# Performance work log

Measured on AMD Instinct MI355X. Metric: run time of the kernel, lower is better.

## Reference

```python
import jax, jax.numpy as jnp
import numpy as np
from jax import lax

# LRN hyperparameters (from module __init__)
K = 2.0
KERNEL = 5
ALPHA = 1e-4
BETA = 0.75
PAD = KERNEL // 2


def setup_inputs() -> dict:
    key = jax.random.key(0)
    x = jax.random.normal(key, (16, 96, 224, 224), dtype=jnp.float32)
    return {"x": x}


def reference(x) -> jnp.ndarray:
    # Spatial local response norm: per-channel k x k box sum of squares
    # (equivalent to Unfold(kernel, pad=kernel//2) -> view -> square -> sum over window).
    sq = x * x
    ssq = lax.reduce_window(
        sq,
        jnp.float32(0.0),
        lax.add,
        window_dimensions=(1, 1, KERNEL, KERNEL),
        window_strides=(1, 1, 1, 1),
        padding=((0, 0), (0, 0), (PAD, PAD), (PAD, PAD)),
    )
    denom = (K + ALPHA * ssq) ** BETA
    return x / denom
```

## Files before the change

kernel.cpp:

```cpp
#include <hip/hip_runtime.h>


typedef float f4 __attribute__((ext_vector_type(4)));

#define LRN_H 224
#define LRN_W 224
#define LRN_WQ 56
#define LRN_R 4
#define LRN_IN (LRN_R + 4)
#define LRN_SLABS (LRN_H / LRN_R)
#define LRN_PLANE (LRN_H * LRN_W)

__global__ __launch_bounds__(256, 6) void LocalResponseNorm_17420387352942_kernel(
        const float* __restrict__ x, float* __restrict__ out) {
    const int q    = threadIdx.x & 63;
    const int wave = threadIdx.x >> 6;
    const int job  = blockIdx.x * 4 + wave;
    const int plane = job / LRN_SLABS;
    const int slab  = job - plane * LRN_SLABS;
    const int h0    = slab * LRN_R;

    const int qe = min(q, LRN_WQ - 1);
    const float* __restrict__ px = x   + (size_t)plane * LRN_PLANE + (qe << 2);
    float* __restrict__       po = out + (size_t)plane * LRN_PLANE + (qe << 2);

    const bool okL = (qe > 0);
    const bool okR = (qe < LRN_WQ - 1);
    const bool wr  = (q < LRN_WQ);

    f4 X[LRN_IN];
#pragma unroll
    for (int r = 0; r < LRN_IN; ++r) {
        const int row = h0 + r - 2;
        const int rc  = min(max(row, 0), LRN_H - 1);
        X[r] = *(const f4*)(px + rc * LRN_W);
    }

    f4 acc[LRN_R];
#pragma unroll
    for (int i = 0; i < LRN_R; ++i) acc[i] = (f4){0.f, 0.f, 0.f, 0.f};

#pragma unroll
    for (int r = 0; r < LRN_IN; ++r) {
        const int row = h0 + r - 2;
        const float mV = (row >= 0 && row < LRN_H) ? 1.0f : 0.0f;
        f4 sq = X[r] * X[r];
        sq *= mV;

        float a  = __shfl_up(sq[2], 1);
        float b  = __shfl_up(sq[3], 1);
        float d0 = __shfl_down(sq[0], 1);
        float d1 = __shfl_down(sq[1], 1);
        a  = okL ? a  : 0.0f;
        b  = okL ? b  : 0.0f;
        d0 = okR ? d0 : 0.0f;
        d1 = okR ? d1 : 0.0f;

        float t = sq[1] + sq[2];
        f4 rs;
        rs[0] = a + b + sq[0] + t;
        rs[1] = b + sq[0] + t + sq[3];
        rs[2] = sq[0] + t + sq[3] + d0;
        rs[3] = t + sq[3] + d0 + d1;

#pragma unroll
        for (int i = 0; i < LRN_R; ++i) {
            if (i <= r && r <= i + 4) acc[i] += rs;
        }
    }

#pragma unroll
    for (int i = 0; i < LRN_R; ++i) {
        f4 o;
#pragma unroll
        for (int j = 0; j < 4; ++j) {
            float d   = fmaf(1e-4f, acc[i][j], 2.0f);
            float rsq = __builtin_amdgcn_rsqf(d);
            o[j] = X[i + 2][j] * rsq * __builtin_amdgcn_sqrtf(rsq);
        }
        if (wr) __builtin_nontemporal_store(o, (f4*)(po + (h0 + i) * LRN_W));
    }
}

extern "C" void kernel_launch(void* const* d_in, const int* in_sizes, int n_in,
                              void* d_out, int out_size, void* d_ws, size_t ws_size,
                              hipStream_t stream) {
    const float* x = (const float*)d_in[0];
    float* out = (float*)d_out;
    dim3 block(256, 1, 1);
    dim3 grid(86016 / 4, 1, 1);
    LocalResponseNorm_17420387352942_kernel<<<grid, block, 0, stream>>>(x, out);
}
```

Before: 512.0 us.

## Halve rows per wave, load horizontal halos directly, swizzle blocks across XCDs

Each wave now produces 2 output rows instead of 4, so the grid doubles, and occupancy is raised to 7 blocks per SIMD. Cross-lane shuffles for the horizontal halo are replaced by extra neighbour vector loads that should hit in cache. Block indices are swizzled so consecutive jobs land on the same XCD, improving L2 locality. The cost is that vertical halo overfetch grows from 8/4 to 6/2 rows per output row, along with extra memory instructions.

```diff
diff --git a/kernel.cpp b/kernel.cpp
--- a/kernel.cpp
+++ b/kernel.cpp
@@ -6,16 +6,20 @@
 #define LRN_H 224
 #define LRN_W 224
 #define LRN_WQ 56
-#define LRN_R 4
+#define LRN_R 2
 #define LRN_IN (LRN_R + 4)
 #define LRN_SLABS (LRN_H / LRN_R)
 #define LRN_PLANE (LRN_H * LRN_W)
+#define LRN_BLOCKS 43008
+#define LRN_BPX (LRN_BLOCKS / 8)
 
-__global__ __launch_bounds__(256, 6) void LocalResponseNorm_17420387352942_kernel(
+__global__ __launch_bounds__(256, 7) void LocalResponseNorm_17420387352942_kernel(
         const float* __restrict__ x, float* __restrict__ out) {
+    const int b    = blockIdx.x;
+    const int swz  = (b & 7) * LRN_BPX + (b >> 3);
     const int q    = threadIdx.x & 63;
     const int wave = threadIdx.x >> 6;
-    const int job  = blockIdx.x * 4 + wave;
+    const int job  = swz * 4 + wave;
     const int plane = job / LRN_SLABS;
     const int slab  = job - plane * LRN_SLABS;
     const int h0    = slab * LRN_R;
@@ -24,61 +28,64 @@
     const float* __restrict__ px = x   + (size_t)plane * LRN_PLANE + (qe << 2);
     float* __restrict__       po = out + (size_t)plane * LRN_PLANE + (qe << 2);
 
-    const bool okL = (qe > 0);
-    const bool okR = (qe < LRN_WQ - 1);
+    const float mL = (qe > 0)          ? 1.0f : 0.0f;
+    const float mR = (qe < LRN_WQ - 1) ? 1.0f : 0.0f;
+    const int offL = (qe > 0)          ? -4 : 0;
+    const int offR = (qe < LRN_WQ - 1) ?  4 : 0;
     const bool wr  = (q < LRN_WQ);
 
-    f4 X[LRN_IN];
+    f4 xc[LRN_IN];
 #pragma unroll
     for (int r = 0; r < LRN_IN; ++r) {
         const int row = h0 + r - 2;
         const int rc  = min(max(row, 0), LRN_H - 1);
-        X[r] = *(const f4*)(px + rc * LRN_W);
+        xc[r] = *(const f4*)(px + rc * LRN_W);
     }
 
-    f4 acc[LRN_R];
-#pragma unroll
-    for (int i = 0; i < LRN_R; ++i) acc[i] = (f4){0.f, 0.f, 0.f, 0.f};
+    f4 acc0 = (f4){0.f, 0.f, 0.f, 0.f};
+    f4 acc1 = (f4){0.f, 0.f, 0.f, 0.f};
 
 #pragma unroll
     for (int r = 0; r < LRN_IN; ++r) {
         const int row = h0 + r - 2;
         const float mV = (row >= 0 && row < LRN_H) ? 1.0f : 0.0f;
-        f4 sq = X[r] * X[r];
-        sq *= mV;
+        const int rc   = min(max(row, 0), LRN_H - 1);
+        const float* rp = px + rc * LRN_W;
+        f4 xl = *(const f4*)(rp + offL);
+        f4 xr = *(const f4*)(rp + offR);
 
-        float a  = __shfl_up(sq[2], 1);
-        float b  = __shfl_up(sq[3], 1);
-        float d0 = __shfl_down(sq[0], 1);
-        float d1 = __shfl_down(sq[1], 1);
-        a  = okL ? a  : 0.0f;
-        b  = okL ? b  : 0.0f;
-        d0 = okR ? d0 : 0.0f;
-        d1 = okR ? d1 : 0.0f;
+        float a  = xl[2] * xl[2] * mL;
+        float bb = xl[3] * xl[3] * mL;
+        float c0 = xc[r][0] * xc[r][0];
+        float c1 = xc[r][1] * xc[r][1];
+        float c2 = xc[r][2] * xc[r][2];
+        float c3 = xc[r][3] * xc[r][3];
+        float d0 = xr[0] * xr[0] * mR;
+        float d1 = xr[1] * xr[1] * mR;
+        float t  = c1 + c2;
+        f4 rs;
+        rs[0] = (a + bb + c0 + t) * mV;
+        rs[1] = (bb + c0 + t + c3) * mV;
+        rs[2] = (c0 + t + c3 + d0) * mV;
+        rs[3] = (t + c3 + d0 + d1) * mV;
 
-        float t = sq[1] + sq[2];
-        f4 rs;
-        rs[0] = a + b + sq[0] + t;
-        rs[1] = b + sq[0] + t + sq[3];
-        rs[2] = sq[0] + t + sq[3] + d0;
-        rs[3] = t + sq[3] + d0 + d1;
-
-#pragma unroll
-        for (int i = 0; i < LRN_R; ++i) {
-            if (i <= r && r <= i + 4) acc[i] += rs;
-        }
+        if (r <= 4) acc0 += rs;
+        if (r >= 1) acc1 += rs;
     }
 
+    f4 o0, o1;
 #pragma unroll
-    for (int i = 0; i < LRN_R; ++i) {
-        f4 o;
-#pragma unroll
-        for (int j = 0; j < 4; ++j) {
-            float d   = fmaf(1e-4f, acc[i][j], 2.0f);
-            float rsq = __builtin_amdgcn_rsqf(d);
-            o[j] = X[i + 2][j] * rsq * __builtin_amdgcn_sqrtf(rsq);
-        }
-        if (wr) __builtin_nontemporal_store(o, (f4*)(po + (h0 + i) * LRN_W));
+    for (int j = 0; j < 4; ++j) {
+        float d0  = fmaf(1e-4f, acc0[j], 2.0f);
+        float rs0 = __builtin_amdgcn_rsqf(d0);
+        o0[j] = xc[2][j] * rs0 * __builtin_amdgcn_sqrtf(rs0);
+        float d1  = fmaf(1e-4f, acc1[j], 2.0f);
+        float rs1 = __builtin_amdgcn_rsqf(d1);
+        o1[j] = xc[3][j] * rs1 * __builtin_amdgcn_sqrtf(rs1);
+    }
+    if (wr) {
+        __builtin_nontemporal_store(o0, (f4*)(po + h0 * LRN_W));
+        __builtin_nontemporal_store(o1, (f4*)(po + (h0 + 1) * LRN_W));
     }
 }
 
@@ -88,6 +95,6 @@
     const float* x = (const float*)d_in[0];
     float* out = (float*)d_out;
     dim3 block(256, 1, 1);
-    dim3 grid(86016 / 4, 1, 1);
+    dim3 grid(LRN_BLOCKS, 1, 1);
     LocalResponseNorm_17420387352942_kernel<<<grid, block, 0, stream>>>(x, out);
 }
```

New measurement: 559.7 us. +9.3%, slower.
